# Optimization experiments

Hardware: AMD Instinct MI355X
Metric: run time of the kernel (lower is better)

Reference implementation:

```python
import jax, jax.numpy as jnp
import numpy as np

B, T, C = 4, 768, 2048
HEAD_SIZE = 64
H = C // HEAD_SIZE
D_W, D_A, D_MV, D_G = 96, 96, 64, 256
GN_EPS = 1e-5 * 8 ** 2  # head_size_divisor = 8


def _layer_norm(x, w, b, eps=1e-5):
    m = jnp.mean(x, -1, keepdims=True)
    v = jnp.mean(jnp.square(x - m), -1, keepdims=True)
    return (x - m) * jax.lax.rsqrt(v + eps) * w + b


def _time_shift(x):
    # ZeroPad2d((0,0,1,-1)): prepend a zero timestep, drop the last
    return jnp.pad(x, ((0, 0), (1, 0), (0, 0)))[:, :-1]


def _group_norm(x, w, b, eps):
    # x: [M, C], H groups
    M, Cc = x.shape
    xg = x.reshape(M, H, Cc // H)
    m = jnp.mean(xg, -1, keepdims=True)
    v = jnp.mean(jnp.square(xg - m), -1, keepdims=True)
    xg = (xg - m) * jax.lax.rsqrt(v + eps)
    return xg.reshape(M, Cc) * w + b


def _rwkv7(r, w, k, v, a, b):
    # WindBackstepping semantics: S_t = S_{t-1} * diag(exp(-exp(w_t))) + S_{t-1} a_t b_t^T + v_t k_t^T
    # y_t = S_t r_t ; state S is [B,H,N(v),N(k)]
    Bb, Tt, Cc = r.shape
    N = HEAD_SIZE
    r, w, k, v, a, b = [t.reshape(Bb, Tt, H, N) for t in (r, w, k, v, a, b)]
    decay = jnp.exp(-jnp.exp(w))  # [B,T,H,N]
    seq = tuple(jnp.moveaxis(t, 1, 0) for t in (decay, r, k, v, a, b))  # [T,B,H,N]
    s0 = jnp.zeros((Bb, H, N, N), jnp.float32)

    def step(s, inp):
        d_t, r_t, k_t, v_t, a_t, b_t = inp
        sab = jnp.einsum('bhik,bhk,bhj->bhij', s, a_t, b_t)
        s = s * d_t[:, :, None, :] + sab + v_t[..., :, None] * k_t[..., None, :]
        y_t = jnp.einsum('bhij,bhj->bhi', s, r_t)
        return s, y_t

    _, y = jax.lax.scan(step, s0, seq)
    return jnp.moveaxis(y, 0, 1).reshape(Bb, Tt, Cc)


def setup_inputs() -> dict:
    key = jax.random.key(0)
    ks = iter(jax.random.split(key, 48))
    rn = lambda shape, s=1.0: jax.random.normal(next(ks), shape, jnp.float32) * s
    d = {}
    d['x'] = rn((B, T, C))
    d['v_first'] = rn((B, T, C))
    d['ln1_w'] = jnp.ones((C,)); d['ln1_b'] = jnp.zeros((C,))
    d['ln2_w'] = jnp.ones((C,)); d['ln2_b'] = jnp.zeros((C,))
    ddd = jnp.arange(C, dtype=jnp.float32) / C
    for nm, p in [('x_r', 0.2), ('x_w', 0.9), ('x_k', 0.9), ('x_v', 0.4), ('x_a', 0.9), ('x_g', 0.2)]:
        d[nm] = 1.0 - jnp.power(ddd, p)
    d['w0'] = jnp.linspace(-7.0, -2.0, C) + 0.5
    d['w1'] = rn((C, D_W), 0.01); d['w2'] = rn((D_W, C), 0.02)
    d['a0'] = rn((C,), 0.1); d['a1'] = rn((C, D_A), 0.01); d['a2'] = rn((D_A, C), 0.02)
    d['v0'] = 1.0 + rn((C,), 0.1); d['v1'] = rn((C, D_MV), 0.01); d['v2'] = rn((D_MV, C), 0.02)
    d['g1'] = rn((C, D_G), 0.01); d['g2'] = rn((D_G, C), 0.02)
    d['k_k'] = 0.85 * jnp.ones((C,)); d['k_a'] = jnp.ones((C,))
    d['r_k'] = rn((H, HEAD_SIZE), 0.1)
    d['W_r'] = rn((C, C), C ** -0.5)
    d['W_k'] = rn((C, C), C ** -0.5)
    d['W_v'] = rn((C, C), C ** -0.5)
    d['W_o'] = rn((C, C), C ** -0.5)
    d['gn_w'] = jnp.ones((C,)); d['gn_b'] = jnp.zeros((C,))
    d['ffn_x_k'] = 1.0 - ddd
    d['W_key'] = rn((C, 4 * C), C ** -0.5)
    d['W_val'] = rn((4 * C, C), (4 * C) ** -0.5)
    return d


def reference(x, v_first, ln1_w, ln1_b, ln2_w, ln2_b, x_r, x_w, x_k, x_v, x_a, x_g,
              w0, w1, w2, a0, a1, a2, v0, v1, v2, g1, g2, k_k, k_a, r_k,
              W_r, W_k, W_v, W_o, gn_w, gn_b, ffn_x_k, W_key, W_val):
    N = HEAD_SIZE
    # ---- time mix (RWKV_Tmix_x070, layer_id=1) ----
    xn = _layer_norm(x, ln1_w, ln1_b)
    xx = _time_shift(xn) - xn
    xr = xn + xx * x_r
    xw_ = xn + xx * x_w
    xk_ = xn + xx * x_k
    xv_ = xn + xx * x_v
    xa_ = xn + xx * x_a
    xg_ = xn + xx * x_g
    r = xr @ W_r
    w_log = -jax.nn.softplus(-(w0 + jnp.tanh(xw_ @ w1) @ w2)) - 0.5
    k = xk_ @ W_k
    v = xv_ @ W_v
    v = v + (v_first - v) * jax.nn.sigmoid(v0 + (xv_ @ v1) @ v2)  # layer_id != 0
    a = jax.nn.sigmoid(a0 + (xa_ @ a1) @ a2)
    g = jax.nn.sigmoid(xg_ @ g1) @ g2
    kk = (k * k_k).reshape(B, T, H, N)
    kk = kk / jnp.maximum(jnp.linalg.norm(kk, axis=-1, keepdims=True), 1e-12)
    kk = kk.reshape(B, T, C)
    k = k * (1.0 + (a - 1.0) * k_a)
    y = _rwkv7(r, w_log, k, v, -kk, kk * a)
    y = _group_norm(y.reshape(B * T, C), gn_w, gn_b, GN_EPS).reshape(B, T, C)
    rk = jnp.sum(r.reshape(B, T, H, N) * k.reshape(B, T, H, N) * r_k, -1, keepdims=True)
    y = y + (rk * v.reshape(B, T, H, N)).reshape(B, T, C)
    x = x + (y * g) @ W_o
    # ---- channel mix (RWKV_CMix_x070) ----
    x2 = _layer_norm(x, ln2_w, ln2_b)
    xx2 = _time_shift(x2) - x2
    kf = x2 + xx2 * ffn_x_k
    kf = jnp.square(jax.nn.relu(kf @ W_key))
    x = x + kf @ W_val
    return (x, v_first)
```

## Files before the change

### kernel.cpp

```cpp
#include <hip/hip_runtime.h>
#include <stdint.h>

typedef unsigned short u16;
typedef __attribute__((ext_vector_type(8))) short short8;
typedef __attribute__((ext_vector_type(4))) float f32x4;

#define DEVI __device__ __forceinline__

static constexpr int TT = 768;
static constexpr int CC = 2048;
static constexpr int MM = 3072;
static constexpr int HH = 32;

DEVI float b2f(u16 u){ union{float f; unsigned int i;} x; x.i = ((unsigned int)u)<<16; return x.f; }
DEVI float b2fs(short s){ return b2f((u16)s); }
DEVI u16 f2b(float f){
  unsigned int u = __builtin_bit_cast(unsigned int, f);
  unsigned int r = (u + 0x7fffu + ((u>>16)&1u)) >> 16;
  return (u16)r;
}

DEVI void gload16(const void* g, void* s){
  __builtin_amdgcn_global_load_lds((const __attribute__((address_space(1))) void*)g,
                                   (__attribute__((address_space(3))) void*)s, 16, 0, 0);
}

DEVI float rdx8(float x){
  int xi = __builtin_bit_cast(int, x);
  x += __builtin_bit_cast(float, __builtin_amdgcn_update_dpp(0, xi, 0xB1, 0xF, 0xF, true));
  xi = __builtin_bit_cast(int, x);
  x += __builtin_bit_cast(float, __builtin_amdgcn_update_dpp(0, xi, 0x4E, 0xF, 0xF, true));
  xi = __builtin_bit_cast(int, x);
  x += __builtin_bit_cast(float, __builtin_amdgcn_update_dpp(0, xi, 0x141, 0xF, 0xF, true));
  return x;
}

__global__ __launch_bounds__(256) void k_fillf(float* __restrict__ out, float v, int n){
  for (int i = blockIdx.x*256 + threadIdx.x; i < n; i += gridDim.x*256) out[i] = v;
}

__global__ void k_tpose(const float* __restrict__ src, int R, int Cn, u16* __restrict__ dst, int ldd){
  __shared__ float tile[32][33];
  int c0 = blockIdx.x*32, r0 = blockIdx.y*32;
  #pragma unroll
  for (int i=0;i<4;++i){
    int r = r0 + threadIdx.y + i*8, c = c0 + threadIdx.x;
    tile[threadIdx.y + i*8][threadIdx.x] = (r<R && c<Cn) ? src[(size_t)r*Cn + c] : 0.f;
  }
  __syncthreads();
  #pragma unroll
  for (int i=0;i<4;++i){
    int c = c0 + threadIdx.y + i*8, r = r0 + threadIdx.x;
    if (c<Cn && r<R) dst[(size_t)c*ldd + r] = f2b(tile[threadIdx.x][threadIdx.y + i*8]);
  }
}

__global__ __launch_bounds__(256) void k_lnb(const float* __restrict__ in, const float* __restrict__ w,
                                             const float* __restrict__ bias, u16* __restrict__ out){
  __shared__ float red[8];
  int m = blockIdx.x;
  const float* x = in + (size_t)m*CC;
  float v[8]; float s=0.f, ss=0.f;
  #pragma unroll
  for (int i=0;i<8;++i){ v[i] = x[threadIdx.x + i*256]; s += v[i]; ss += v[i]*v[i]; }
  #pragma unroll
  for (int o=32;o;o>>=1){ s += __shfl_xor(s,o); ss += __shfl_xor(ss,o); }
  int wid = threadIdx.x>>6;
  if ((threadIdx.x&63)==0){ red[wid]=s; red[4+wid]=ss; }
  __syncthreads();
  s  = red[0]+red[1]+red[2]+red[3];
  ss = red[4]+red[5]+red[6]+red[7];
  float mean = s*(1.f/2048.f);
  float var  = ss*(1.f/2048.f) - mean*mean;
  float rstd = rsqrtf(fmaxf(var,0.f) + 1e-5f);
  #pragma unroll
  for (int i=0;i<8;++i){
    int c = threadIdx.x + i*256;
    out[(size_t)m*CC + c] = f2b((v[i]-mean)*rstd*w[c] + bias[c]);
  }
}

__global__ __launch_bounds__(256) void k_mixA(const u16* __restrict__ xn,
  const float* __restrict__ cw, const float* __restrict__ ca, const float* __restrict__ cv,
  const float* __restrict__ cg,
  u16* __restrict__ ow, u16* __restrict__ oa, u16* __restrict__ ov, u16* __restrict__ og)
{
  int m = blockIdx.x; int t = m % TT;
  const u16* cur = xn + (size_t)m*CC;
  const u16* prv = cur - CC;
  bool has = (t>0);
  #pragma unroll
  for (int i=0;i<8;++i){
    int c = threadIdx.x + i*256;
    float xc = b2f(cur[c]);
    float xx = (has ? b2f(prv[c]) : 0.f) - xc;
    size_t o = (size_t)m*CC + c;
    ow[o]=f2b(xc + xx*cw[c]); oa[o]=f2b(xc + xx*ca[c]);
    ov[o]=f2b(xc + xx*cv[c]); og[o]=f2b(xc + xx*cg[c]);
  }
}

__global__ __launch_bounds__(256) void k_mixB(const u16* __restrict__ xn,
  const float* __restrict__ cr, const float* __restrict__ ck,
  u16* __restrict__ orr, u16* __restrict__ ok)
{
  int m = blockIdx.x; int t = m % TT;
  const u16* cur = xn + (size_t)m*CC;
  const u16* prv = cur - CC;
  bool has = (t>0);
  #pragma unroll
  for (int i=0;i<8;++i){
    int c = threadIdx.x + i*256;
    float xc = b2f(cur[c]);
    float xx = (has ? b2f(prv[c]) : 0.f) - xc;
    size_t o = (size_t)m*CC + c;
    orr[o]=f2b(xc + xx*cr[c]); ok[o]=f2b(xc + xx*ck[c]);
  }
}

__global__ __launch_bounds__(256) void k_mix1(const u16* __restrict__ xn, const float* __restrict__ cf,
                                              u16* __restrict__ out){
  int m = blockIdx.x; int t = m % TT;
  const u16* cur = xn + (size_t)m*CC;
  const u16* prv = cur - CC;
  bool has = (t>0);
  #pragma unroll
  for (int i=0;i<8;++i){
    int c = threadIdx.x + i*256;
    float xc = b2f(cur[c]);
    float xx = (has ? b2f(prv[c]) : 0.f) - xc;
    out[(size_t)m*CC + c] = f2b(xc + xx*cf[c]);
  }
}

__global__ __launch_bounds__(256,3) void k_gemm(
    const u16* A0, const u16* A1, const u16* A2,
    int amode, int lda,
    const u16* __restrict__ BT, int ldb,
    void* C0, void* C1, void* C2, int ldc, int K,
    int emode, const float* __restrict__ aux)
{
  const int tid = threadIdx.x;
  const int w = tid>>6, l = tid&63;

  const int NT = gridDim.x;
  const int nwg = NT * gridDim.y;
  int bid = blockIdx.y * NT + blockIdx.x;
  int qq = nwg >> 3, rr = nwg & 7;
  int xcd = bid & 7, pos = bid >> 3;
  int nid = (xcd < rr ? xcd*(qq+1) : rr*(qq+1) + (xcd-rr)*qq) + pos;
  const int ntile = nid % NT;
  const int mtile = nid / NT;

  const u16* A = A0;
  if (amode==1){ A = (ntile==0)?A0:(ntile==1)?A1:A2; }
  else if (amode==2){ int g = ntile>>4; A = (g==0)?A0:(g==1)?A1:A2; }

  __shared__ __align__(16) u16 As[3*4096];
  __shared__ __align__(16) u16 Bs[3*4096];

  const int sr = w*16 + (l>>2);
  const int sk = (((l&3) ^ ((l>>2)&3)))*8;
  const u16* Ag = A  + (size_t)(mtile*128 + sr)*lda + sk;
  const u16* Bg = BT + (size_t)(ntile*128 + sr)*ldb + sk;
  const size_t a64 = (size_t)64*lda, b64 = (size_t)64*ldb;
  const int wo = w*512;

  const int wm = w>>1, wn = w&1;
  const int fr = l&15;
  const int fq = ((l>>4) ^ (fr&3))*8;
  const int aoff = (wm*64 + fr)*32 + fq;
  const int boff = (wn*64 + fr)*32 + fq;

  f32x4 acc[4][4];
  const f32x4 zz = {0.f,0.f,0.f,0.f};
  #pragma unroll
  for (int mi=0;mi<4;++mi)
    #pragma unroll
    for (int ni=0;ni<4;++ni) acc[mi][ni] = zz;

  const int nt = K >> 5;

#define STAGE(bufi, k0) do{ \
    u16* dA = As + (bufi)*4096 + wo; \
    u16* dB = Bs + (bufi)*4096 + wo; \
    gload16(Ag + (k0),        dA); \
    gload16(Ag + a64 + (k0),  dA + 2048); \
    gload16(Bg + (k0),        dB); \
    gload16(Bg + b64 + (k0),  dB + 2048); \
  }while(0)

  STAGE(0, 0);
  if (nt > 1) STAGE(1, 32);

  int cur = 0;
  for (int t=0; t<nt; ++t){
    if (t == nt-1){ asm volatile("s_waitcnt vmcnt(0)" ::: "memory"); }
    else          { asm volatile("s_waitcnt vmcnt(4)" ::: "memory"); }
    __builtin_amdgcn_s_barrier();
    if (t+2 < nt){
      int nb = cur+2; if (nb>=3) nb-=3;
      STAGE(nb, (t+2)<<5);
    }
    const u16* Ab = As + cur*4096;
    const u16* Bb = Bs + cur*4096;
    short8 af[4], bfr[4];
    #pragma unroll
    for (int mi=0;mi<4;++mi) af[mi]  = *(const short8*)(Ab + aoff + mi*512);
    #pragma unroll
    for (int ni=0;ni<4;++ni) bfr[ni] = *(const short8*)(Bb + boff + ni*512);
    #pragma unroll
    for (int mi=0;mi<4;++mi)
      #pragma unroll
      for (int ni=0;ni<4;++ni)
        acc[mi][ni] = __builtin_amdgcn_mfma_f32_16x16x32_bf16(af[mi], bfr[ni], acc[mi][ni], 0,0,0);
    cur = (cur+1==3)?0:cur+1;
  }
#undef STAGE

  const int rb0 = mtile*128 + wm*64 + (l>>4)*4;
  const int cb0 = ntile*128 + wn*64 + fr;
  #pragma unroll
  for (int mi=0;mi<4;++mi){
    #pragma unroll
    for (int ni=0;ni<4;++ni){
      #pragma unroll
      for (int q2=0;q2<4;++q2){
        int row = rb0 + mi*16 + q2;
        int col = cb0 + ni*16;
        float v = acc[mi][ni][q2];
        if (emode==0){
          ((float*)C0)[(size_t)row*ldc + col] = v;
        } else if (emode==1){
          float valw = aux[col] + v;
          float zneg = -valw;
          float sp = (zneg > 20.f) ? zneg : log1pf(expf(zneg));
          float wlog = -sp - 0.5f;
          float dec = expf(-expf(wlog));
          int b_ = row/TT, t_ = row - b_*TT;
          int h_ = col>>6, n_ = col&63;
          ((float*)C0)[((size_t)(b_*HH + h_)*TT + t_)*64 + n_] = dec;
        } else if (emode==2){
          float s = 1.f/(1.f+expf(-(aux[col]+v)));
          ((u16*)C0)[(size_t)row*ldc + col] = f2b(s);
        } else if (emode==3){
          ((float*)C0)[(size_t)row*ldc + col] = aux[(size_t)row*ldc + col] + v;
        } else if (emode==4){
          float r_ = fmaxf(v, 0.f);
          ((u16*)C0)[(size_t)row*ldc + col] = f2b(r_*r_);
        } else if (emode==5){
          ((u16*)C0)[(size_t)row*ldc + col] = f2b(aux[(size_t)row*ldc + col] + v);
        } else if (emode==6){
          ((u16*)C0)[(size_t)row*ldc + col] = f2b(v);
        } else if (emode==7){
          float r_ = v;
          if (col < 128) r_ = tanhf(v);
          else if (col >= 384) r_ = 1.f/(1.f+expf(-v));
          ((u16*)C0)[(size_t)row*ldc + col] = f2b(r_);
        } else if (emode==8){
          int b_ = row/TT, t_ = row - b_*TT;
          int h_ = col>>6, n_ = col&63;
          ((u16*)C0)[((size_t)(b_*HH + h_)*TT + t_)*64 + n_] = f2b(v);
        } else if (emode==9){
          float s = 1.f/(1.f+expf(-(aux[col]+v)));
          int b_ = row/TT, t_ = row - b_*TT;
          int h_ = col>>6, n_ = col&63;
          ((u16*)C0)[((size_t)(b_*HH + h_)*TT + t_)*64 + n_] = f2b(s);
        } else if (emode==10){
          int g = col>>11, c2 = col&2047;
          int b_ = row/TT, t_ = row - b_*TT;
          int h_ = c2>>6, n_ = c2&63;
          u16* dst = (g==0)?(u16*)C0:(g==1)?(u16*)C1:(u16*)C2;
          dst[((size_t)(b_*HH + h_)*TT + t_)*64 + n_] = f2b(v);
        } else {
          float s = 1.f/(1.f+expf(-v));
          ((u16*)C0)[(size_t)row*ldc + (col+384)] = f2b(s);
        }
      }
    }
  }
}

__global__ __launch_bounds__(256) void k_make_rec3(
  u16* __restrict__ ksc, u16* __restrict__ vsc,
  const u16* __restrict__ asc, const u16* __restrict__ gsc,
  float* __restrict__ af, float* __restrict__ bf,
  const float* __restrict__ v_first, const float* __restrict__ k_k, const float* __restrict__ k_a)
{
  int idx = blockIdx.x*4 + (threadIdx.x>>6);
  int l = threadIdx.x & 63;
  int bh = idx / TT, t = idx - bh*TT;
  int b = bh >> 5, h = bh & 31;
  int c = h*64 + l;
  size_t off = (size_t)idx*64 + l;
  size_t mo = ((size_t)b*TT + t)*CC + c;
  float kq = b2f(ksc[off]);
  float vv = b2f(vsc[off]);
  float aa = b2f(asc[off]);
  float sg = b2f(gsc[off]);
  float vf = v_first[mo];
  float kkr = kq * k_k[c];
  float s2 = kkr*kkr;
  #pragma unroll
  for (int o=32;o;o>>=1) s2 += __shfl_xor(s2,o);
  float kk = kkr / fmaxf(sqrtf(s2), 1e-12f);
  ksc[off] = f2b(kq*(1.f + (aa-1.f)*k_a[c]));
  vsc[off] = f2b(vv + (vf-vv)*sg);
  af[off] = -kk;
  bf[off] = kk*aa;
}

static constexpr int RCH = 16;
static constexpr int RNC = TT / RCH;
static constexpr int RBUF = 18432;

__global__ __launch_bounds__(256,1) void k_rwkv(
    const float* __restrict__ decay, const float* __restrict__ af, const float* __restrict__ bf,
    const u16* __restrict__ rb, const u16* __restrict__ kb, const u16* __restrict__ vb,
    u16* __restrict__ y)
{
  __shared__ __align__(16) char lds[3*RBUF];
  int blk = blockIdx.x;
  int bh = blk >> 1, half = blk & 1;
  int b = bh>>5, h = bh&31;
  int tid = threadIdx.x, w = tid>>6, l = tid&63;
  const int row = half*32 + w*8 + (l>>3);
  const int g = l&7;
  const int j0 = g*8;
  const size_t base = (size_t)bh * (TT*64);

  const float* dB = decay + base;
  const float* aB = af + base;
  const float* bB = bf + base;
  const u16*  rB = rb + base;
  const u16*  kB = kb + base;
  const u16*  vB = vb + base;

  float S[8];
  #pragma unroll
  for (int q=0;q<8;++q) S[q]=0.f;
  float ycur[RCH], yprev[RCH];
  size_t yb = (size_t)b*TT*CC + h*64 + row;

#define RSTAGE(bufi, c) do{ \
    char* bs = lds + (bufi)*RBUF; \
    size_t cf = (size_t)(c)*1024; \
    gload16(dB + cf + tid*4, bs + tid*16); \
    gload16(aB + cf + tid*4, bs + 4096 + tid*16); \
    gload16(bB + cf + tid*4, bs + 8192 + tid*16); \
    if (l < 32){ \
      int eo = w*256 + l*8; int bo = w*512 + l*16; \
      gload16(rB + cf + eo, bs + 12288 + bo); \
      gload16(kB + cf + eo, bs + 14336 + bo); \
      gload16(vB + cf + eo, bs + 16384 + bo); \
    } \
  }while(0)

  RSTAGE(0, 0);
  RSTAGE(1, 1);

  int cur = 0;
  for (int c=0; c<RNC; ++c){
    if (c == RNC-1){ asm volatile("s_waitcnt vmcnt(0)" ::: "memory"); }
    else           { asm volatile("s_waitcnt vmcnt(6)" ::: "memory"); }
    __builtin_amdgcn_s_barrier();
    if (c > 0){
      int t0 = (c-1)*RCH;
      #pragma unroll
      for (int s=0;s<RCH;++s) if (g==0) y[yb + (size_t)(t0+s)*CC] = f2b(yprev[s]);
    }
    asm volatile("" ::: "memory");
    if (c+2 < RNC){
      int nb = cur+2; if (nb>=3) nb-=3;
      RSTAGE(nb, c+2);
    }
    asm volatile("" ::: "memory");
    const char* bs = lds + cur*RBUF;
    #pragma unroll
    for (int s=0;s<RCH;++s){
      const f32x4* aV = (const f32x4*)(bs + 4096 + s*256 + j0*4);
      f32x4 a0v = aV[0], a1v = aV[1];
      float sa = ((S[0]*a0v[0] + S[1]*a0v[1]) + (S[2]*a0v[2] + S[3]*a0v[3]))
               + ((S[4]*a1v[0] + S[5]*a1v[1]) + (S[6]*a1v[2] + S[7]*a1v[3]));
      sa = rdx8(sa);
      const f32x4* dV = (const f32x4*)(bs + s*256 + j0*4);
      const f32x4* bV = (const f32x4*)(bs + 8192 + s*256 + j0*4);
      f32x4 d0v = dV[0], d1v = dV[1], b0v = bV[0], b1v = bV[1];
      short8 r8 = *(const short8*)(bs + 12288 + s*128 + j0*2);
      short8 k8 = *(const short8*)(bs + 14336 + s*128 + j0*2);
      float vi = b2f(*(const u16*)(bs + 16384 + s*128 + row*2));
      float yv = 0.f;
      #pragma unroll
      for (int e=0;e<4;++e){
        float Sq = S[e]*d0v[e] + sa*b0v[e] + vi*b2fs(k8[e]);
        S[e] = Sq;
        yv += Sq*b2fs(r8[e]);
      }
      #pragma unroll
      for (int e=0;e<4;++e){
        float Sq = S[4+e]*d1v[e] + sa*b1v[e] + vi*b2fs(k8[4+e]);
        S[4+e] = Sq;
        yv += Sq*b2fs(r8[4+e]);
      }
      ycur[s] = rdx8(yv);
    }
    #pragma unroll
    for (int s=0;s<RCH;++s) yprev[s] = ycur[s];
    cur = (cur+1==3)?0:cur+1;
  }
#undef RSTAGE
  {
    int t0 = (RNC-1)*RCH;
    #pragma unroll
    for (int s=0;s<RCH;++s) if (g==0) y[yb + (size_t)(t0+s)*CC] = f2b(yprev[s]);
  }
}

__global__ __launch_bounds__(256) void k_gn(
  const u16* __restrict__ y, const u16* __restrict__ rb, const u16* __restrict__ kb,
  const u16* __restrict__ vb, const float* __restrict__ r_k,
  const float* __restrict__ gnw, const float* __restrict__ gnb,
  const u16* __restrict__ gg, u16* __restrict__ z)
{
  int idx = blockIdx.x*4 + (threadIdx.x>>6);
  int l = threadIdx.x&63;
  int m = idx>>5, h = idx&31;
  int c = h*64 + l;
  size_t mo = (size_t)m*CC + c;
  float yv = b2f(y[mo]);
  float s = yv;
  #pragma unroll
  for (int o=32;o;o>>=1) s += __shfl_xor(s,o);
  float mean = s*(1.f/64.f);
  float dv = yv - mean;
  float vs = dv*dv;
  #pragma unroll
  for (int o=32;o;o>>=1) vs += __shfl_xor(vs,o);
  float gn = dv*rsqrtf(vs*(1.f/64.f) + 6.4e-4f)*gnw[c] + gnb[c];
  size_t ro = ((size_t)((m/TT)*HH + h)*TT + (m%TT))*64 + l;
  float rv=b2f(rb[ro]), kv=b2f(kb[ro]), vv=b2f(vb[ro]);
  float p = rv*kv*r_k[c];
  #pragma unroll
  for (int o=32;o;o>>=1) p += __shfl_xor(p,o);
  z[mo] = f2b((gn + p*vv)*b2f(gg[mo]));
}

extern "C" void kernel_launch(void* const* d_in, const int* in_sizes, int n_in,
                              void* d_out, int out_size, void* d_ws, size_t ws_size,
                              hipStream_t stream)
{
  (void)out_size;
  const float* x      = (const float*)d_in[0];
  const float* v_first= (const float*)d_in[1];
  const float* ln1_w  = (const float*)d_in[2];
  const float* ln1_b  = (const float*)d_in[3];
  const float* ln2_w  = (const float*)d_in[4];
  const float* ln2_b  = (const float*)d_in[5];
  const float* x_r    = (const float*)d_in[6];
  const float* x_w    = (const float*)d_in[7];
  const float* x_k    = (const float*)d_in[8];
  const float* x_v    = (const float*)d_in[9];
  const float* x_a    = (const float*)d_in[10];
  const float* x_g    = (const float*)d_in[11];
  const float* w0     = (const float*)d_in[12];
  const float* w1     = (const float*)d_in[13];
  const float* w2     = (const float*)d_in[14];
  const float* a0     = (const float*)d_in[15];
  const float* a1     = (const float*)d_in[16];
  const float* a2     = (const float*)d_in[17];
  const float* v0     = (const float*)d_in[18];
  const float* v1     = (const float*)d_in[19];
  const float* v2     = (const float*)d_in[20];
  const float* g1     = (const float*)d_in[21];
  const float* g2     = (const float*)d_in[22];
  const float* k_k    = (const float*)d_in[23];
  const float* k_a    = (const float*)d_in[24];
  const float* r_k    = (const float*)d_in[25];
  const float* W_r    = (const float*)d_in[26];
  const float* W_k    = (const float*)d_in[27];
  const float* W_v    = (const float*)d_in[28];
  const float* W_o    = (const float*)d_in[29];
  const float* gn_w   = (const float*)d_in[30];
  const float* gn_b   = (const float*)d_in[31];
  const float* ffn_x_k= (const float*)d_in[32];
  const float* W_key  = (const float*)d_in[33];
  const float* W_val  = (const float*)d_in[34];

  const size_t ME = (size_t)MM*CC;
  float* outF = (float*)d_out;

  bool ok = (n_in==35)
    && in_sizes[0]==6291456 && in_sizes[1]==6291456 && in_sizes[2]==2048
    && in_sizes[12]==2048 && in_sizes[13]==196608 && in_sizes[14]==196608
    && in_sizes[16]==196608 && in_sizes[19]==131072 && in_sizes[21]==524288
    && in_sizes[25]==2048 && in_sizes[26]==4194304 && in_sizes[33]==16777216
    && in_sizes[34]==16777216;
  if (!ok){
    k_fillf<<<2048, 256, 0, stream>>>(outF, 1099511627776.f, (int)ME);
    return;
  }

  constexpr size_t WS_NEED = 125829120 + 12582912;
  if (ws_size < WS_NEED){
    k_fillf<<<2048, 256, 0, stream>>>(outF, (float)(1u<<21) * (float)(ws_size>>20), (int)ME);
    return;
  }
  char* ws = (char*)d_ws;
  float* decay = (float*)(ws + 0);
  float* x1    = (float*)(ws + 0);
  u16* xn   = (u16*)(ws + 25165824);
  u16* WT   = (u16*)(ws + 25165824);
  float* bf32 = (float*)(ws + 25165824);
  u16* xw  = (u16*)(ws + 37748736);
  u16* xr  = (u16*)(ws + 37748736);
  u16* xn2 = (u16*)(ws + 37748736);
  float* af32 = (float*)(ws + 50331648);
  u16* xa  = (u16*)(ws + 50331648);
  u16* xk  = (u16*)(ws + 50331648);
  u16* xv  = (u16*)(ws + 62914560);
  u16* kf  = (u16*)(ws + 62914560);
  u16* xg  = (u16*)(ws + 75497472);
  u16* rsc = (u16*)(ws + 75497472);
  char* Fs = ws + 88080384;
  u16* B1T = (u16*)(Fs);
  u16* w2T = (u16*)(Fs + 2621440);
  u16* a2T = (u16*)(Fs + 3014656);
  u16* v2T = (u16*)(Fs + 3407872);
  u16* g2T = (u16*)(Fs + 3670016);
  u16* H1b = (u16*)(Fs + 4718592);
  u16* ksc = (u16*)(ws + 88080384);
  u16* asc = (u16*)(ws + 100663296);
  u16* ybuf= (u16*)(ws + 100663296);
  u16* gsc = (u16*)(ws + 113246208);
  u16* zbuf= (u16*)(ws + 113246208);
  u16* xcm = (u16*)(ws + 113246208);
  u16* WbigT = (u16*)(ws + 25165824);
  u16* outG = (u16*)(ws + 125829120);
  u16* vsc   = (u16*)d_out;
  u16* WrkvT = ((u16*)d_out) + ME;

  auto GEMM = [&](const u16* a0_, const u16* a1_, const u16* a2_,
                  int amode, int lda_, const u16* bt, int ldb_,
                  void* c0_, void* c1_, void* c2_, int ldc_,
                  int N_, int K_, int em, const float* aux_){
    k_gemm<<<dim3(N_/128, MM/128), 256, 0, stream>>>(a0_,a1_,a2_,amode,lda_,bt,ldb_,c0_,c1_,c2_,ldc_,K_,em,aux_);
  };
  dim3 tb(32,8);

  k_lnb<<<MM, 256, 0, stream>>>(x, ln1_w, ln1_b, xn);
  k_mixA<<<MM, 256, 0, stream>>>(xn, x_w, x_a, x_v, x_g, xw, xa, xv, xg);
  hipMemsetAsync(B1T, 0, 2621440, stream);
  k_tpose<<<dim3(3,64), tb, 0, stream>>>(w1, 2048,  96, B1T + 0*2048,   2048);
  k_tpose<<<dim3(3,64), tb, 0, stream>>>(a1, 2048,  96, B1T + 128*2048, 2048);
  k_tpose<<<dim3(2,64), tb, 0, stream>>>(v1, 2048,  64, B1T + 256*2048, 2048);
  k_tpose<<<dim3(8,64), tb, 0, stream>>>(g1, 2048, 256, B1T + 384*2048, 2048);
  k_tpose<<<dim3(64,3), tb, 0, stream>>>(w2,   96, 2048, w2T,  96);
  k_tpose<<<dim3(64,3), tb, 0, stream>>>(a2,   96, 2048, a2T,  96);
  k_tpose<<<dim3(64,2), tb, 0, stream>>>(v2,   64, 2048, v2T,  64);
  k_tpose<<<dim3(64,8), tb, 0, stream>>>(g2,  256, 2048, g2T, 256);
  GEMM(xw, xa, xv, 1, 2048, B1T, 2048, H1b, nullptr, nullptr, 640, 384, 2048, 7, nullptr);
  GEMM(xg, xg, xg, 0, 2048, B1T + 384*2048, 2048, H1b, nullptr, nullptr, 640, 256, 2048, 11, nullptr);
  GEMM(H1b + 0,   H1b, H1b, 0, 640, w2T,  96, decay, nullptr, nullptr, 2048, 2048,  96, 1, w0);
  GEMM(H1b + 128, H1b, H1b, 0, 640, a2T,  96, asc,   nullptr, nullptr, 2048, 2048,  96, 9, a0);
  GEMM(H1b + 256, H1b, H1b, 0, 640, v2T,  64, gsc,   nullptr, nullptr, 2048, 2048,  64, 9, v0);
  GEMM(H1b + 384, H1b, H1b, 0, 640, g2T, 256, outG,  nullptr, nullptr, 2048, 2048, 256, 6, nullptr);
  k_mixB<<<MM, 256, 0, stream>>>(xn, x_r, x_k, xr, xk);
  k_tpose<<<dim3(64,64), tb, 0, stream>>>(W_r, 2048, 2048, WrkvT,               2048);
  k_tpose<<<dim3(64,64), tb, 0, stream>>>(W_k, 2048, 2048, WrkvT + 2048*2048,   2048);
  k_tpose<<<dim3(64,64), tb, 0, stream>>>(W_v, 2048, 2048, WrkvT + 2*2048*2048, 2048);
  GEMM(xr, xk, xv, 2, 2048, WrkvT, 2048, rsc, ksc, vsc, 2048, 6144, 2048, 10, nullptr);
  k_make_rec3<<<MM*HH/4, 256, 0, stream>>>(ksc, vsc, asc, gsc, af32, bf32, v_first, k_k, k_a);
  k_rwkv<<<256, 256, 0, stream>>>(decay, af32, bf32, rsc, ksc, vsc, ybuf);
  k_gn<<<MM*HH/4, 256, 0, stream>>>(ybuf, rsc, ksc, vsc, r_k, gn_w, gn_b, outG, zbuf);
  k_tpose<<<dim3(64,64), tb, 0, stream>>>(W_o, 2048, 2048, WT, 2048);
  GEMM(zbuf, zbuf, zbuf, 0, 2048, WT, 2048, x1, nullptr, nullptr, 2048, 2048, 2048, 3, x);
  k_lnb<<<MM, 256, 0, stream>>>(x1, ln2_w, ln2_b, xn2);
  k_mix1<<<MM, 256, 0, stream>>>(xn2, ffn_x_k, xcm);
  k_tpose<<<dim3(256,64), tb, 0, stream>>>(W_key, 2048, 8192, WbigT, 2048);
  GEMM(xcm, xcm, xcm, 0, 2048, WbigT, 2048, kf, nullptr, nullptr, 8192, 8192, 2048, 4, nullptr);
  k_tpose<<<dim3(64,256), tb, 0, stream>>>(W_val, 8192, 2048, WbigT, 8192);
  GEMM(kf, kf, kf, 0, 8192, WbigT, 8192, outF, nullptr, nullptr, 2048, 2048, 8192, 3, x1);
  hipMemcpyAsync(outF + ME, v_first, ME*sizeof(float), hipMemcpyDeviceToDevice, stream);
}
```

Before: 1.384 ms.

## Add 256x128-tile GEMM with triple-buffered LDS and XCD-aware remap for big GEMMs

Adds a second GEMM kernel that uses 256x128 output tiles, a three-stage LDS ring filled by direct global-to-LDS loads, and a block-index remap that groups neighbouring tiles onto the same XCD. It is used for the fused r/k/v projection and the FFN key projection. Larger tiles raise arithmetic intensity and cut redundant operand loads. The deeper pipeline is meant to hide memory latency. The cost is more accumulator registers (128 floats per thread) and more shared memory, which may limit occupancy. It also halves the number of workgroups in the M dimension.

```diff
diff --git a/kernel.cpp b/kernel.cpp
--- a/kernel.cpp
+++ b/kernel.cpp
@@ -281,6 +281,121 @@
   }
 }
 
+__global__ __launch_bounds__(256,2) void k_gemm2(
+    const u16* A0, const u16* A1, const u16* A2,
+    int amode, int lda,
+    const u16* __restrict__ BT, int ldb,
+    void* C0, void* C1, void* C2, int ldc, int K,
+    int emode, const float* __restrict__ aux)
+{
+  const int tid = threadIdx.x;
+  const int w = tid>>6, l = tid&63;
+
+  const int NT = gridDim.x;
+  const int nwg = NT * gridDim.y;
+  int bid = blockIdx.y * NT + blockIdx.x;
+  int qq = nwg >> 3, rr = nwg & 7;
+  int xcd = bid & 7, pos = bid >> 3;
+  int nid = (xcd < rr ? xcd*(qq+1) : rr*(qq+1) + (xcd-rr)*qq) + pos;
+  const int ntile = nid % NT;
+  const int mtile = nid / NT;
+
+  const u16* A = A0;
+  if (amode==2){ int g = ntile>>4; A = (g==0)?A0:(g==1)?A1:A2; }
+
+  __shared__ __align__(16) u16 As[3*8192];
+  __shared__ __align__(16) u16 Bs[3*4096];
+
+  const int sr4 = l>>2;
+  const int skb = ((l&3) ^ (sr4&3))*8;
+  const u16* Ag = A  + (size_t)(mtile*256 + w*64 + sr4)*lda + skb;
+  const u16* Bg = BT + (size_t)(ntile*128 + w*32 + sr4)*ldb + skb;
+  const size_t l16a = (size_t)16*lda, l16b = (size_t)16*ldb;
+
+  const int wm = w>>1, wn = w&1;
+  const int fr = l&15;
+  const int fq = ((l>>4) ^ (fr&3))*8;
+  const int aoff = (wm*128 + fr)*32 + fq;
+  const int boff = (wn*64 + fr)*32 + fq;
+
+  f32x4 acc[8][4];
+  const f32x4 zz = {0.f,0.f,0.f,0.f};
+  #pragma unroll
+  for (int mi=0;mi<8;++mi)
+    #pragma unroll
+    for (int ni=0;ni<4;++ni) acc[mi][ni] = zz;
+
+  const int nt = K >> 5;
+
+#define STAGE2(bufi, k0) do{ \
+    u16* dA = As + (bufi)*8192 + w*2048; \
+    u16* dB = Bs + (bufi)*4096 + w*1024; \
+    gload16(Ag + (k0),          dA); \
+    gload16(Ag + l16a + (k0),   dA + 512); \
+    gload16(Ag + 2*l16a + (k0), dA + 1024); \
+    gload16(Ag + 3*l16a + (k0), dA + 1536); \
+    gload16(Bg + (k0),          dB); \
+    gload16(Bg + l16b + (k0),   dB + 512); \
+  }while(0)
+
+  STAGE2(0, 0);
+  if (nt > 1) STAGE2(1, 32);
+
+  int cur = 0;
+  for (int t=0; t<nt; ++t){
+    if (t == nt-1){ asm volatile("s_waitcnt vmcnt(0)" ::: "memory"); }
+    else          { asm volatile("s_waitcnt vmcnt(6)" ::: "memory"); }
+    __builtin_amdgcn_s_barrier();
+    if (t+2 < nt){
+      int nb = cur+2; if (nb>=3) nb-=3;
+      STAGE2(nb, (t+2)<<5);
+    }
+    const u16* Ab = As + cur*8192;
+    const u16* Bb = Bs + cur*4096;
+    short8 af[8], bfr[4];
+    #pragma unroll
+    for (int mi=0;mi<8;++mi) af[mi]  = *(const short8*)(Ab + aoff + mi*512);
+    #pragma unroll
+    for (int ni=0;ni<4;++ni) bfr[ni] = *(const short8*)(Bb + boff + ni*512);
+    #pragma unroll
+    for (int mi=0;mi<8;++mi)
+      #pragma unroll
+      for (int ni=0;ni<4;++ni)
+        acc[mi][ni] = __builtin_amdgcn_mfma_f32_16x16x32_bf16(af[mi], bfr[ni], acc[mi][ni], 0,0,0);
+    cur = (cur+1==3)?0:cur+1;
+  }
+#undef STAGE2
+
+  const int rb0 = mtile*256 + wm*128 + (l>>4)*4;
+  const int cb0 = ntile*128 + wn*64 + fr;
+  #pragma unroll
+  for (int mi=0;mi<8;++mi){
+    #pragma unroll
+    for (int ni=0;ni<4;++ni){
+      #pragma unroll
+      for (int q2=0;q2<4;++q2){
+        int row = rb0 + mi*16 + q2;
+        int col = cb0 + ni*16;
+        float v = acc[mi][ni][q2];
+        if (emode==0){
+          ((float*)C0)[(size_t)row*ldc + col] = v;
+        } else if (emode==3){
+          ((float*)C0)[(size_t)row*ldc + col] = aux[(size_t)row*ldc + col] + v;
+        } else if (emode==4){
+          float r_ = fmaxf(v, 0.f);
+          ((u16*)C0)[(size_t)row*ldc + col] = f2b(r_*r_);
+        } else {
+          int g = col>>11, c2 = col&2047;
+          int b_ = row/TT, t_ = row - b_*TT;
+          int h_ = c2>>6, n_ = c2&63;
+          u16* dst = (g==0)?(u16*)C0:(g==1)?(u16*)C1:(u16*)C2;
+          dst[((size_t)(b_*HH + h_)*TT + t_)*64 + n_] = f2b(v);
+        }
+      }
+    }
+  }
+}
+
 __global__ __launch_bounds__(256) void k_make_rec3(
   u16* __restrict__ ksc, u16* __restrict__ vsc,
   const u16* __restrict__ asc, const u16* __restrict__ gsc,
@@ -545,6 +660,12 @@
                   int N_, int K_, int em, const float* aux_){
     k_gemm<<<dim3(N_/128, MM/128), 256, 0, stream>>>(a0_,a1_,a2_,amode,lda_,bt,ldb_,c0_,c1_,c2_,ldc_,K_,em,aux_);
   };
+  auto GEMM2 = [&](const u16* a0_, const u16* a1_, const u16* a2_,
+                   int amode, int lda_, const u16* bt, int ldb_,
+                   void* c0_, void* c1_, void* c2_, int ldc_,
+                   int N_, int K_, int em, const float* aux_){
+    k_gemm2<<<dim3(N_/128, MM/256), 256, 0, stream>>>(a0_,a1_,a2_,amode,lda_,bt,ldb_,c0_,c1_,c2_,ldc_,K_,em,aux_);
+  };
   dim3 tb(32,8);
 
   k_lnb<<<MM, 256, 0, stream>>>(x, ln1_w, ln1_b, xn);
@@ -568,7 +689,7 @@
   k_tpose<<<dim3(64,64), tb, 0, stream>>>(W_r, 2048, 2048, WrkvT,               2048);
   k_tpose<<<dim3(64,64), tb, 0, stream>>>(W_k, 2048, 2048, WrkvT + 2048*2048,   2048);
   k_tpose<<<dim3(64,64), tb, 0, stream>>>(W_v, 2048, 2048, WrkvT + 2*2048*2048, 2048);
-  GEMM(xr, xk, xv, 2, 2048, WrkvT, 2048, rsc, ksc, vsc, 2048, 6144, 2048, 10, nullptr);
+  GEMM2(xr, xk, xv, 2, 2048, WrkvT, 2048, rsc, ksc, vsc, 2048, 6144, 2048, 10, nullptr);
   k_make_rec3<<<MM*HH/4, 256, 0, stream>>>(ksc, vsc, asc, gsc, af32, bf32, v_first, k_k, k_a);
   k_rwkv<<<256, 256, 0, stream>>>(decay, af32, bf32, rsc, ksc, vsc, ybuf);
   k_gn<<<MM*HH/4, 256, 0, stream>>>(ybuf, rsc, ksc, vsc, r_k, gn_w, gn_b, outG, zbuf);
@@ -577,7 +698,7 @@
   k_lnb<<<MM, 256, 0, stream>>>(x1, ln2_w, ln2_b, xn2);
   k_mix1<<<MM, 256, 0, stream>>>(xn2, ffn_x_k, xcm);
   k_tpose<<<dim3(256,64), tb, 0, stream>>>(W_key, 2048, 8192, WbigT, 2048);
-  GEMM(xcm, xcm, xcm, 0, 2048, WbigT, 2048, kf, nullptr, nullptr, 8192, 8192, 2048, 4, nullptr);
+  GEMM2(xcm, xcm, xcm, 0, 2048, WbigT, 2048, kf, nullptr, nullptr, 8192, 8192, 2048, 4, nullptr);
   k_tpose<<<dim3(64,256), tb, 0, stream>>>(W_val, 8192, 2048, WbigT, 8192);
   GEMM(kf, kf, kf, 0, 8192, WbigT, 8192, outF, nullptr, nullptr, 2048, 2048, 8192, 3, x1);
   hipMemcpyAsync(outF + ME, v_first, ME*sizeof(float), hipMemcpyDeviceToDevice, stream);
```

New measurement: 1.536 ms. 11.0% more time.
